# Optimization experiments

Measured on AMD Instinct MI355X. Metric: run time of the kernel, lower is better.

## Reference

```python
import jax, jax.numpy as jnp
import numpy as np

B, S, D, H = 2, 2048, 2048, 16
HD = D // H  # head_dim = 128


def setup_inputs() -> dict:
    key = jax.random.key(0)
    ks = jax.random.split(key, 5)
    scale = 1.0 / np.sqrt(D)
    return {
        "x": jax.random.normal(ks[0], (B, S, D), dtype=jnp.float32),
        "Wq": jax.random.normal(ks[1], (D, D), dtype=jnp.float32) * scale,
        "Wk": jax.random.normal(ks[2], (D, D), dtype=jnp.float32) * scale,
        "Wv": jax.random.normal(ks[3], (D, D), dtype=jnp.float32) * scale,
        "Wo": jax.random.normal(ks[4], (D, D), dtype=jnp.float32) * scale,
    }


def reference(x, Wq, Wk, Wv, Wo):
    # torch Linear: y = x @ W.T (weight is [out, in], no bias)
    b, s, d = x.shape
    def split_heads(t):
        return t.reshape(b, s, H, HD).transpose(0, 2, 1, 3)  # [B,H,S,HD]
    q = split_heads(x @ Wq.T)
    k = split_heads(x @ Wk.T)
    v = split_heads(x @ Wv.T)
    scores = jnp.einsum("bhqd,bhkd->bhqk", q, k) / jnp.sqrt(jnp.float32(HD))
    attn = jax.nn.softmax(scores, axis=-1)
    out = jnp.einsum("bhqk,bhkd->bhqd", attn, v)  # [B,H,S,HD]
    out = out.transpose(0, 2, 1, 3).reshape(b, s, d)
    return out @ Wo.T
```

## Files before the change

### kernel.cpp

```cpp
#include <hip/hip_runtime.h>
#include <stdint.h>

typedef unsigned short u16t;
typedef short bf16x8 __attribute__((ext_vector_type(8)));
typedef float f32x4 __attribute__((ext_vector_type(4)));

#define B_ 2
#define S_ 2048
#define D_ 2048
#define H_ 16
#define HD_ 128

#define MFMA16(a,b,c) __builtin_amdgcn_mfma_f32_16x16x32_bf16((a),(b),(c),0,0,0)

typedef const __attribute__((address_space(1))) void* gptr_t;
typedef __attribute__((address_space(3))) void* lptr_t;
#define GLL16(src, dst) __builtin_amdgcn_global_load_lds((gptr_t)(src), (lptr_t)(dst), 16, 0, 0)

__device__ __forceinline__ u16t f2bf(float f) {
  uint32_t u = __builtin_bit_cast(uint32_t, f);
  u = (u + 0x7fffu + ((u >> 16) & 1u)) >> 16;
  return (u16t)u;
}

__global__ void cvt_kernel(const float* __restrict__ in, u16t* __restrict__ out, int n8) {
  int i = blockIdx.x * blockDim.x + threadIdx.x;
  if (i >= n8) return;
  const float4* p = (const float4*)in + (size_t)i * 2;
  float4 a = p[0], b = p[1];
  union { u16t u[8]; uint4 v; } pk;
  pk.u[0]=f2bf(a.x); pk.u[1]=f2bf(a.y); pk.u[2]=f2bf(a.z); pk.u[3]=f2bf(a.w);
  pk.u[4]=f2bf(b.x); pk.u[5]=f2bf(b.y); pk.u[6]=f2bf(b.z); pk.u[7]=f2bf(b.w);
  *(uint4*)(out + (size_t)i * 8) = pk.v;
}

__global__ void wcvt_kernel(const float* __restrict__ w0, const float* __restrict__ w1,
                            const float* __restrict__ w2, const float* __restrict__ w3,
                            u16t* o0, u16t* o1, u16t* o2, u16t* o3) {
  int blk = blockIdx.x;
  int wsel = blk >> 11;
  const float* in = (wsel == 0) ? w0 : (wsel == 1) ? w1 : (wsel == 2) ? w2 : w3;
  u16t* out = (wsel == 0) ? o0 : (wsel == 1) ? o1 : (wsel == 2) ? o2 : o3;
  int i = (blk & 2047) * 256 + threadIdx.x;
  const float4* p = (const float4*)in + (size_t)i * 2;
  float4 a = p[0], b = p[1];
  union { u16t u[8]; uint4 v; } pk;
  pk.u[0]=f2bf(a.x); pk.u[1]=f2bf(a.y); pk.u[2]=f2bf(a.z); pk.u[3]=f2bf(a.w);
  pk.u[4]=f2bf(b.x); pk.u[5]=f2bf(b.y); pk.u[6]=f2bf(b.z); pk.u[7]=f2bf(b.w);
  *(uint4*)(out + (size_t)i * 8) = pk.v;
}

template<int OUT_BF16>
__global__ __launch_bounds__(512, 2) void gemm256(const u16t* __restrict__ A,
                                                  const u16t* __restrict__ Bw0,
                                                  const u16t* __restrict__ Bw1,
                                                  const u16t* __restrict__ Bw2,
                                                  void* __restrict__ C0,
                                                  void* __restrict__ C1,
                                                  void* __restrict__ C2,
                                                  int Mtiles, int Ntiles, int tpw,
                                                  int K, float a0, float a1, float a2) {
  __shared__ __attribute__((aligned(16))) u16t Al[2][2][128*64];
  __shared__ __attribute__((aligned(16))) u16t Bl[2][2][128*64];
  int nwg = Mtiles * Ntiles;
  int bid = blockIdx.x;
  int wg  = ((bid & 7) * (nwg >> 3)) + (bid >> 3);
  int mt = wg / Ntiles, nt = wg % Ntiles;
  int wsel = nt / tpw;
  const u16t* Bw = (wsel == 0) ? Bw0 : (wsel == 1) ? Bw1 : Bw2;
  const u16t* Ag = A  + (size_t)mt * 256 * K;
  const u16t* Bg = Bw + (size_t)(nt - wsel*tpw) * 256 * K;

  int t = threadIdx.x, lane = t & 63, w = t >> 6;
  int wm = w >> 2, wn = w & 3;
  int c = lane & 15, g = lane >> 4;

  auto stageA = [&](int buf, int hf, int kt) {
    #pragma unroll
    for (int j = 0; j < 2; j++) {
      int s = j*512 + t;
      int row = s >> 3;
      int ks = (s & 7) ^ (row & 7);
      GLL16(Ag + (size_t)(hf*128 + row) * K + kt*64 + ks*8,
            &Al[buf][hf][(j*512 + (t & ~63)) * 8]);
    }
  };
  auto stageB = [&](int buf, int hf, int kt) {
    #pragma unroll
    for (int j = 0; j < 2; j++) {
      int s = j*512 + t;
      int row = s >> 3;
      int ks = (s & 7) ^ (row & 7);
      GLL16(Bg + (size_t)(hf*128 + row) * K + kt*64 + ks*8,
            &Bl[buf][hf][(j*512 + (t & ~63)) * 8]);
    }
  };

  f32x4 acc[8][4];
  #pragma unroll
  for (int mf = 0; mf < 8; mf++)
    #pragma unroll
    for (int nf = 0; nf < 4; nf++) acc[mf][nf] = (f32x4){0.f,0.f,0.f,0.f};

  int nk = K >> 6;
  stageA(0,0,0); stageA(0,1,0); stageB(0,0,0); stageB(0,1,0);
  stageA(1,0,1); stageA(1,1,1); stageB(1,0,1); stageB(1,1,1);

  int sAo[2];
  #pragma unroll
  for (int ks = 0; ks < 2; ks++) sAo[ks] = (((ks*4 + g) ^ (c & 7)) << 3);
  int arow = c * 64;
  int brow = ((wn & 1) * 64 + c) * 64;

  bf16x8 Af[8][2], Bf[4][2];
  auto quad = [&](int MF0, int NF0) {
    __builtin_amdgcn_s_setprio(1);
    #pragma unroll
    for (int mq = 0; mq < 4; mq++)
      #pragma unroll
      for (int nq = 0; nq < 2; nq++)
        #pragma unroll
        for (int ks = 0; ks < 2; ks++)
          acc[MF0+mq][NF0+nq] = MFMA16(Af[MF0+mq][ks], Bf[NF0+nq][ks], acc[MF0+mq][NF0+nq]);
    __builtin_amdgcn_s_setprio(0);
  };

  for (int kt = 0; kt < nk; ++kt) {
    int p = kt & 1;
    if (kt < nk - 1) asm volatile("s_waitcnt vmcnt(8)" ::: "memory");
    else             asm volatile("s_waitcnt vmcnt(0)" ::: "memory");
    __builtin_amdgcn_s_barrier();
    #pragma unroll
    for (int mf = 0; mf < 8; mf++)
      #pragma unroll
      for (int ks = 0; ks < 2; ks++)
        Af[mf][ks] = *(const bf16x8*)&Al[p][wm][mf*1024 + arow + sAo[ks]];
    #pragma unroll
    for (int nf = 0; nf < 4; nf++)
      #pragma unroll
      for (int ks = 0; ks < 2; ks++)
        Bf[nf][ks] = *(const bf16x8*)&Bl[p][wn >> 1][nf*1024 + brow + sAo[ks]];
    quad(0, 0);
    asm volatile("s_waitcnt lgkmcnt(0)" ::: "memory");
    __builtin_amdgcn_s_barrier();
    if (kt + 2 < nk) { stageA(p, 0, kt + 2); stageA(p, 1, kt + 2); }
    quad(0, 2);
    __builtin_amdgcn_s_barrier();
    if (kt + 2 < nk) { stageB(p, 0, kt + 2); stageB(p, 1, kt + 2); }
    quad(4, 0);
    __builtin_amdgcn_s_barrier();
    quad(4, 2);
  }

  float alpha = (wsel == 0) ? a0 : (wsel == 1) ? a1 : a2;
  void* Cv = (wsel == 0) ? C0 : (wsel == 1) ? C1 : C2;
  int m0 = mt*256 + wm*128 + 4*g;
  int n0 = (nt - wsel*tpw)*256 + wn*64 + c;
  if (OUT_BF16) {
    u16t* C = (u16t*)Cv;
    #pragma unroll
    for (int mf = 0; mf < 8; mf++)
      #pragma unroll
      for (int nf = 0; nf < 4; nf++)
        #pragma unroll
        for (int r = 0; r < 4; r++)
          C[(size_t)(m0 + 16*mf + r) * D_ + n0 + 16*nf] = f2bf(acc[mf][nf][r] * alpha);
  } else {
    float* C = (float*)Cv;
    #pragma unroll
    for (int mf = 0; mf < 8; mf++)
      #pragma unroll
      for (int nf = 0; nf < 4; nf++)
        #pragma unroll
        for (int r = 0; r < 4; r++)
          C[(size_t)(m0 + 16*mf + r) * D_ + n0 + 16*nf] = acc[mf][nf][r] * alpha;
  }
}

__global__ void vtrans_kernel(const u16t* __restrict__ V, u16t* __restrict__ Vt) {
  __shared__ __attribute__((aligned(16))) u16t T[64][72];
  int bid = blockIdx.x;
  int dt = bid & 1;
  int st = (bid >> 1) & 31;
  int head = bid >> 6;
  int b = head >> 4, h = head & 15;
  int t = threadIdx.x;
  #pragma unroll
  for (int p = 0; p < 2; p++) {
    int sr = p*32 + (t >> 3), x = t & 7;
    uint4 v = *(const uint4*)&V[(size_t)(b*S_ + st*64 + sr)*D_ + h*HD_ + dt*64 + x*8];
    *(uint4*)&T[sr][x*8] = v;
  }
  __syncthreads();
  #pragma unroll
  for (int p = 0; p < 2; p++) {
    int dr = p*32 + (t >> 3), x = t & 7;
    union { u16t u[8]; uint4 v; } pk;
    #pragma unroll
    for (int j = 0; j < 8; j++) pk.u[j] = T[x*8 + j][dr];
    *(uint4*)&Vt[(size_t)(head*HD_ + dt*64 + dr)*S_ + st*64 + x*8] = pk.v;
  }
}

__global__ __launch_bounds__(256, 2) void attn_kernel(const u16t* __restrict__ Q,
                                                      const u16t* __restrict__ Kg,
                                                      const u16t* __restrict__ Vt,
                                                      u16t* __restrict__ O) {
  __shared__ __attribute__((aligned(16))) u16t Kl[2][64*128];
  __shared__ __attribute__((aligned(16))) u16t Vl[2][128*64];
  __shared__ __attribute__((aligned(16))) u16t Pl[4][32*64];
  int bid = blockIdx.x;
  int qt = bid & 15, head = bid >> 4;
  int b = head >> 4, h = head & 15;
  int t = threadIdx.x, lane = t & 63, w = t >> 6;
  int c = lane & 15, g = lane >> 4;
  int q0 = qt*128 + w*32;

  bf16x8 qf[2][4];
  #pragma unroll
  for (int mi = 0; mi < 2; mi++)
    #pragma unroll
    for (int ks = 0; ks < 4; ks++)
      qf[mi][ks] = *(const bf16x8*)&Q[(size_t)(b*S_ + q0 + c + 16*mi)*D_ + h*HD_ + 8*g + 32*ks];

  f32x4 oacc[8][2];
  #pragma unroll
  for (int mf = 0; mf < 8; mf++) { oacc[mf][0] = (f32x4){0,0,0,0}; oacc[mf][1] = (f32x4){0,0,0,0}; }
  f32x4 lacc[2];
  lacc[0] = (f32x4){0,0,0,0}; lacc[1] = (f32x4){0,0,0,0};
  bf16x8 ones;
  #pragma unroll
  for (int j = 0; j < 8; j++) ones[j] = (short)0x3F80;

  auto stageK = [&](int buf, int kt) {
    int s0 = kt*64;
    #pragma unroll
    for (int i = 0; i < 4; i++) {
      int row = (i*256 + t) >> 4;
      int xs = (t & 15) ^ (row & 15);
      GLL16(&Kg[(size_t)(b*S_ + s0 + row)*D_ + h*HD_ + xs*8], &Kl[buf][(i*256 + (t & ~63))*8]);
    }
  };
  auto stageV = [&](int buf, int kt) {
    int s0 = kt*64;
    #pragma unroll
    for (int i = 0; i < 4; i++) {
      int d = (i*256 + t) >> 3;
      int xs = (t & 7) ^ (d & 7);
      GLL16(&Vt[(size_t)(head*HD_ + d)*S_ + s0 + xs*8], &Vl[buf][(i*256 + (t & ~63))*8]);
    }
  };

  stageK(0, 0); stageV(0, 0);
  int cur = 0;
  for (int kt = 0; kt < 32; ++kt) {
    __syncthreads();
    if (kt + 1 < 32) { stageK(cur ^ 1, kt + 1); stageV(cur ^ 1, kt + 1); }

    f32x4 sacc[2][4];
    #pragma unroll
    for (int mi = 0; mi < 2; mi++)
      #pragma unroll
      for (int nf = 0; nf < 4; nf++) sacc[mi][nf] = (f32x4){0,0,0,0};
    #pragma unroll
    for (int ks = 0; ks < 4; ks++) {
      #pragma unroll
      for (int nf = 0; nf < 4; nf++) {
        bf16x8 kf = *(const bf16x8*)&Kl[cur][(c + 16*nf)*128 + (((g + 4*ks) ^ c) & 15)*8];
        sacc[0][nf] = MFMA16(qf[0][ks], kf, sacc[0][nf]);
        sacc[1][nf] = MFMA16(qf[1][ks], kf, sacc[1][nf]);
      }
    }

    #pragma unroll
    for (int mi = 0; mi < 2; mi++)
      #pragma unroll
      for (int nf = 0; nf < 4; nf++)
        #pragma unroll
        for (int reg = 0; reg < 4; reg++) {
          float p = __expf(sacc[mi][nf][reg]);
          int r = 16*mi + 4*g + reg;
          int col = c + 16*nf;
          Pl[w][r*64 + ((((col >> 3) ^ (r & 7)) & 7) << 3) + (col & 7)] = f2bf(p);
        }

    #pragma unroll
    for (int ks = 0; ks < 2; ks++) {
      int ps = ((g + 4*ks) ^ (c & 7)) & 7;
      bf16x8 pf0 = *(const bf16x8*)&Pl[w][(c      )*64 + ps*8];
      bf16x8 pf1 = *(const bf16x8*)&Pl[w][(c + 16 )*64 + ps*8];
      lacc[0] = MFMA16(ones, pf0, lacc[0]);
      lacc[1] = MFMA16(ones, pf1, lacc[1]);
      #pragma unroll
      for (int mf = 0; mf < 8; mf++) {
        bf16x8 vf = *(const bf16x8*)&Vl[cur][(c + 16*mf)*64 + ps*8];
        oacc[mf][0] = MFMA16(vf, pf0, oacc[mf][0]);
        oacc[mf][1] = MFMA16(vf, pf1, oacc[mf][1]);
      }
    }
    cur ^= 1;
  }

  float li0 = 1.f / lacc[0][0];
  float li1 = 1.f / lacc[1][0];
  #pragma unroll
  for (int mf = 0; mf < 8; mf++) {
    #pragma unroll
    for (int nf = 0; nf < 2; nf++) {
      float liv = nf ? li1 : li0;
      union { u16t u[4]; uint2 v; } pk;
      #pragma unroll
      for (int r = 0; r < 4; r++) pk.u[r] = f2bf(oacc[mf][nf][r] * liv);
      int qrow = q0 + c + 16*nf;
      int d0 = 16*mf + 4*g;
      *(uint2*)&O[(size_t)(b*S_ + qrow)*D_ + h*HD_ + d0] = pk.v;
    }
  }
}

extern "C" void kernel_launch(void* const* d_in, const int* in_sizes, int n_in,
                              void* d_out, int out_size, void* d_ws, size_t ws_size,
                              hipStream_t stream) {
  const float* x  = (const float*)d_in[0];
  const float* Wq = (const float*)d_in[1];
  const float* Wk = (const float*)d_in[2];
  const float* Wv = (const float*)d_in[3];
  const float* Wo = (const float*)d_in[4];

  const size_t M1 = 1024*1024;
  u16t* ws  = (u16t*)d_ws;
  u16t* xb  = ws;
  u16t* Wqb = xb  + 8*M1;
  u16t* Wkb = Wqb + 4*M1;
  u16t* Wvb = Wkb + 4*M1;
  u16t* Wob = Wvb + 4*M1;
  u16t* Qb  = Wob + 4*M1;
  u16t* Vb  = (u16t*)d_out;
  u16t* Kb  = (u16t*)d_out + 8*M1;
  u16t* Vtb = xb;
  u16t* AOb = Wqb;

  const float scl = 0.08838834764831845f;

  cvt_kernel<<<4096, 256, 0, stream>>>(x, xb, 1048576);
  wcvt_kernel<<<8192, 256, 0, stream>>>(Wq, Wk, Wv, Wo, Wqb, Wkb, Wvb, Wob);

  gemm256<1><<<384, 512, 0, stream>>>(xb, Wqb, Wkb, Wvb, Qb, Kb, Vb,
                                      16, 24, 8, 2048, scl, 1.0f, 1.0f);

  vtrans_kernel<<<2048, 256, 0, stream>>>(Vb, Vtb);

  attn_kernel<<<512, 256, 0, stream>>>(Qb, Kb, Vtb, AOb);

  gemm256<0><<<128, 512, 0, stream>>>(AOb, Wob, Wob, Wob, d_out, d_out, d_out,
                                      16, 8, 8, 2048, 1.0f, 1.0f, 1.0f);
}
```

Baseline: 393.4 us.

## Fuse conversions, write V transposed from GEMM epilogue, restructure GEMM pipeline

Merges the x and weight fp32-to-bf16 conversion kernels into a single launch. The QKV GEMM epilogue now writes V directly in transposed layout, which removes the separate vtrans kernel and its extra round trip through memory. The GEMM main loop is also rewritten into a finer-grained software pipeline: it unrolls over two k-tiles and interleaves partial LDS reads, global-to-LDS staging and MFMA quads, with more barriers in exchange. The transposed V stores are 8-byte scattered writes, which may coalesce worse than the old per-element row writes.

```diff
diff --git a/kernel.cpp b/kernel.cpp
--- a/kernel.cpp
+++ b/kernel.cpp
@@ -23,9 +23,20 @@
   return (u16t)u;
 }
 
-__global__ void cvt_kernel(const float* __restrict__ in, u16t* __restrict__ out, int n8) {
-  int i = blockIdx.x * blockDim.x + threadIdx.x;
-  if (i >= n8) return;
+__global__ void cvt5_kernel(const float* __restrict__ x,
+                            const float* __restrict__ w0, const float* __restrict__ w1,
+                            const float* __restrict__ w2, const float* __restrict__ w3,
+                            u16t* xo, u16t* o0, u16t* o1, u16t* o2, u16t* o3) {
+  int blk = blockIdx.x;
+  const float* in; u16t* out; int i;
+  if (blk < 4096) { in = x; out = xo; i = blk * 256 + threadIdx.x; }
+  else {
+    int b2 = blk - 4096;
+    int wsel = b2 >> 11;
+    in  = (wsel == 0) ? w0 : (wsel == 1) ? w1 : (wsel == 2) ? w2 : w3;
+    out = (wsel == 0) ? o0 : (wsel == 1) ? o1 : (wsel == 2) ? o2 : o3;
+    i = (b2 & 2047) * 256 + threadIdx.x;
+  }
   const float4* p = (const float4*)in + (size_t)i * 2;
   float4 a = p[0], b = p[1];
   union { u16t u[8]; uint4 v; } pk;
@@ -34,23 +45,7 @@
   *(uint4*)(out + (size_t)i * 8) = pk.v;
 }
 
-__global__ void wcvt_kernel(const float* __restrict__ w0, const float* __restrict__ w1,
-                            const float* __restrict__ w2, const float* __restrict__ w3,
-                            u16t* o0, u16t* o1, u16t* o2, u16t* o3) {
-  int blk = blockIdx.x;
-  int wsel = blk >> 11;
-  const float* in = (wsel == 0) ? w0 : (wsel == 1) ? w1 : (wsel == 2) ? w2 : w3;
-  u16t* out = (wsel == 0) ? o0 : (wsel == 1) ? o1 : (wsel == 2) ? o2 : o3;
-  int i = (blk & 2047) * 256 + threadIdx.x;
-  const float4* p = (const float4*)in + (size_t)i * 2;
-  float4 a = p[0], b = p[1];
-  union { u16t u[8]; uint4 v; } pk;
-  pk.u[0]=f2bf(a.x); pk.u[1]=f2bf(a.y); pk.u[2]=f2bf(a.z); pk.u[3]=f2bf(a.w);
-  pk.u[4]=f2bf(b.x); pk.u[5]=f2bf(b.y); pk.u[6]=f2bf(b.z); pk.u[7]=f2bf(b.w);
-  *(uint4*)(out + (size_t)i * 8) = pk.v;
-}
-
-template<int OUT_BF16>
+template<int MODE>
 __global__ __launch_bounds__(512, 2) void gemm256(const u16t* __restrict__ A,
                                                   const u16t* __restrict__ Bw0,
                                                   const u16t* __restrict__ Bw1,
@@ -102,17 +97,27 @@
     #pragma unroll
     for (int nf = 0; nf < 4; nf++) acc[mf][nf] = (f32x4){0.f,0.f,0.f,0.f};
 
-  int nk = K >> 6;
-  stageA(0,0,0); stageA(0,1,0); stageB(0,0,0); stageB(0,1,0);
-  stageA(1,0,1); stageA(1,1,1); stageB(1,0,1); stageB(1,1,1);
-
-  int sAo[2];
-  #pragma unroll
-  for (int ks = 0; ks < 2; ks++) sAo[ks] = (((ks*4 + g) ^ (c & 7)) << 3);
+  int sOf[2];
+  #pragma unroll
+  for (int ks = 0; ks < 2; ks++) sOf[ks] = (((ks*4 + g) ^ (c & 7)) << 3);
   int arow = c * 64;
-  int brow = ((wn & 1) * 64 + c) * 64;
+  int brow = (wn & 1) * 4096 + c * 64;
 
   bf16x8 Af[8][2], Bf[4][2];
+  auto RD_A = [&](int p, int mf0) {
+    #pragma unroll
+    for (int mq = 0; mq < 4; mq++)
+      #pragma unroll
+      for (int ks = 0; ks < 2; ks++)
+        Af[mf0+mq][ks] = *(const bf16x8*)&Al[p][wm][(mf0+mq)*1024 + arow + sOf[ks]];
+  };
+  auto RD_B = [&](int p, int nf0) {
+    #pragma unroll
+    for (int nq = 0; nq < 2; nq++)
+      #pragma unroll
+      for (int ks = 0; ks < 2; ks++)
+        Bf[nf0+nq][ks] = *(const bf16x8*)&Bl[p][wn >> 1][(nf0+nq)*1024 + brow + sOf[ks]];
+  };
   auto quad = [&](int MF0, int NF0) {
     __builtin_amdgcn_s_setprio(1);
     #pragma unroll
@@ -124,40 +129,59 @@
           acc[MF0+mq][NF0+nq] = MFMA16(Af[MF0+mq][ks], Bf[NF0+nq][ks], acc[MF0+mq][NF0+nq]);
     __builtin_amdgcn_s_setprio(0);
   };
-
-  for (int kt = 0; kt < nk; ++kt) {
-    int p = kt & 1;
-    if (kt < nk - 1) asm volatile("s_waitcnt vmcnt(8)" ::: "memory");
-    else             asm volatile("s_waitcnt vmcnt(0)" ::: "memory");
-    __builtin_amdgcn_s_barrier();
-    #pragma unroll
-    for (int mf = 0; mf < 8; mf++)
-      #pragma unroll
-      for (int ks = 0; ks < 2; ks++)
-        Af[mf][ks] = *(const bf16x8*)&Al[p][wm][mf*1024 + arow + sAo[ks]];
-    #pragma unroll
-    for (int nf = 0; nf < 4; nf++)
-      #pragma unroll
-      for (int ks = 0; ks < 2; ks++)
-        Bf[nf][ks] = *(const bf16x8*)&Bl[p][wn >> 1][nf*1024 + brow + sAo[ks]];
-    quad(0, 0);
-    asm volatile("s_waitcnt lgkmcnt(0)" ::: "memory");
-    __builtin_amdgcn_s_barrier();
-    if (kt + 2 < nk) { stageA(p, 0, kt + 2); stageA(p, 1, kt + 2); }
-    quad(0, 2);
-    __builtin_amdgcn_s_barrier();
-    if (kt + 2 < nk) { stageB(p, 0, kt + 2); stageB(p, 1, kt + 2); }
-    quad(4, 0);
-    __builtin_amdgcn_s_barrier();
-    quad(4, 2);
-  }
+  #define BAR() __builtin_amdgcn_s_barrier()
+  #define LGKM0() asm volatile("s_waitcnt lgkmcnt(0)" ::: "memory")
+
+  int nk = K >> 6;
+  stageA(0,0,0); stageA(0,1,0); stageB(0,0,0); stageB(0,1,0);
+  stageA(1,0,1);
+  asm volatile("s_waitcnt vmcnt(2)" ::: "memory");
+  BAR();
+
+  for (int it = 0; it < nk/2; ++it) {
+    int t1 = 2*it + 1, tn0 = 2*it + 2, tn1 = 2*it + 3;
+    bool st = tn0 < nk;
+    RD_A(0,0); RD_B(0,0);
+    stageA(1,1,t1);
+    BAR(); LGKM0(); quad(0,0); BAR();
+    RD_B(0,2);
+    stageB(1,0,t1);
+    BAR(); LGKM0(); quad(0,2); BAR();
+    RD_A(0,4);
+    stageB(1,1,t1);
+    BAR(); LGKM0(); quad(4,0); BAR();
+    if (st) { stageA(0,0,tn0); asm volatile("s_waitcnt vmcnt(2)" ::: "memory"); }
+    else    {                  asm volatile("s_waitcnt vmcnt(0)" ::: "memory"); }
+    BAR(); quad(4,2); BAR();
+    RD_A(1,0); RD_B(1,0);
+    if (st) stageA(0,1,tn0);
+    BAR(); LGKM0(); quad(0,0); BAR();
+    RD_B(1,2);
+    if (st) stageB(0,0,tn0);
+    BAR(); LGKM0(); quad(0,2); BAR();
+    RD_A(1,4);
+    if (st) stageB(0,1,tn0);
+    BAR(); LGKM0(); quad(4,0); BAR();
+    if (st) { stageA(1,0,tn1); asm volatile("s_waitcnt vmcnt(2)" ::: "memory"); }
+    BAR(); quad(4,2); BAR();
+  }
+  #undef BAR
+  #undef LGKM0
 
   float alpha = (wsel == 0) ? a0 : (wsel == 1) ? a1 : a2;
-  void* Cv = (wsel == 0) ? C0 : (wsel == 1) ? C1 : C2;
   int m0 = mt*256 + wm*128 + 4*g;
   int n0 = (nt - wsel*tpw)*256 + wn*64 + c;
-  if (OUT_BF16) {
-    u16t* C = (u16t*)Cv;
+  if (MODE == 0) {
+    float* C = (float*)C0;
+    #pragma unroll
+    for (int mf = 0; mf < 8; mf++)
+      #pragma unroll
+      for (int nf = 0; nf < 4; nf++)
+        #pragma unroll
+        for (int r = 0; r < 4; r++)
+          C[(size_t)(m0 + 16*mf + r) * D_ + n0 + 16*nf] = acc[mf][nf][r] * alpha;
+  } else if (wsel != 2) {
+    u16t* C = (u16t*)((wsel == 0) ? C0 : C1);
     #pragma unroll
     for (int mf = 0; mf < 8; mf++)
       #pragma unroll
@@ -166,39 +190,20 @@
         for (int r = 0; r < 4; r++)
           C[(size_t)(m0 + 16*mf + r) * D_ + n0 + 16*nf] = f2bf(acc[mf][nf][r] * alpha);
   } else {
-    float* C = (float*)Cv;
-    #pragma unroll
-    for (int mf = 0; mf < 8; mf++)
-      #pragma unroll
-      for (int nf = 0; nf < 4; nf++)
-        #pragma unroll
-        for (int r = 0; r < 4; r++)
-          C[(size_t)(m0 + 16*mf + r) * D_ + n0 + 16*nf] = acc[mf][nf][r] * alpha;
-  }
-}
-
-__global__ void vtrans_kernel(const u16t* __restrict__ V, u16t* __restrict__ Vt) {
-  __shared__ __attribute__((aligned(16))) u16t T[64][72];
-  int bid = blockIdx.x;
-  int dt = bid & 1;
-  int st = (bid >> 1) & 31;
-  int head = bid >> 6;
-  int b = head >> 4, h = head & 15;
-  int t = threadIdx.x;
-  #pragma unroll
-  for (int p = 0; p < 2; p++) {
-    int sr = p*32 + (t >> 3), x = t & 7;
-    uint4 v = *(const uint4*)&V[(size_t)(b*S_ + st*64 + sr)*D_ + h*HD_ + dt*64 + x*8];
-    *(uint4*)&T[sr][x*8] = v;
-  }
-  __syncthreads();
-  #pragma unroll
-  for (int p = 0; p < 2; p++) {
-    int dr = p*32 + (t >> 3), x = t & 7;
-    union { u16t u[8]; uint4 v; } pk;
-    #pragma unroll
-    for (int j = 0; j < 8; j++) pk.u[j] = T[x*8 + j][dr];
-    *(uint4*)&Vt[(size_t)(head*HD_ + dt*64 + dr)*S_ + st*64 + x*8] = pk.v;
+    u16t* Vt = (u16t*)C2;
+    #pragma unroll
+    for (int mf = 0; mf < 8; mf++) {
+      int m = m0 + 16*mf;
+      int rowb = (m >> 11) << 11;
+      int colb = m & 2047;
+      #pragma unroll
+      for (int nf = 0; nf < 4; nf++) {
+        union { u16t u[4]; uint2 v; } pk;
+        #pragma unroll
+        for (int r = 0; r < 4; r++) pk.u[r] = f2bf(acc[mf][nf][r] * alpha);
+        *(uint2*)&Vt[(size_t)(rowb + n0 + 16*nf) * 2048 + colb] = pk.v;
+      }
+    }
   }
 }
 
@@ -335,20 +340,16 @@
   u16t* Wvb = Wkb + 4*M1;
   u16t* Wob = Wvb + 4*M1;
   u16t* Qb  = Wob + 4*M1;
-  u16t* Vb  = (u16t*)d_out;
+  u16t* Vtb = (u16t*)d_out;
   u16t* Kb  = (u16t*)d_out + 8*M1;
-  u16t* Vtb = xb;
   u16t* AOb = Wqb;
 
   const float scl = 0.08838834764831845f;
 
-  cvt_kernel<<<4096, 256, 0, stream>>>(x, xb, 1048576);
-  wcvt_kernel<<<8192, 256, 0, stream>>>(Wq, Wk, Wv, Wo, Wqb, Wkb, Wvb, Wob);
-
-  gemm256<1><<<384, 512, 0, stream>>>(xb, Wqb, Wkb, Wvb, Qb, Kb, Vb,
+  cvt5_kernel<<<12288, 256, 0, stream>>>(x, Wq, Wk, Wv, Wo, xb, Wqb, Wkb, Wvb, Wob);
+
+  gemm256<1><<<384, 512, 0, stream>>>(xb, Wqb, Wkb, Wvb, Qb, Kb, Vtb,
                                       16, 24, 8, 2048, scl, 1.0f, 1.0f);
-
-  vtrans_kernel<<<2048, 256, 0, stream>>>(Vb, Vtb);
 
   attn_kernel<<<512, 256, 0, stream>>>(Qb, Kb, Vtb, AOb);
 
```

Result: slower. 407.5 us (+3.6%).
